# Kernel tuning notes

Hardware: AMD Instinct MI355X
Metric: run time of the kernel (lower is better)

Reference implementation:

```python
import jax, jax.numpy as jnp
import numpy as np

T = 32768   # frames
N = 1024    # notes
THRESHOLD = 0.5  # half a semitone (quarter tone) in midi norm


def setup_inputs() -> dict:
    key = jax.random.key(0)
    k1, k2 = jax.random.split(key)
    gen_f0 = jax.random.normal(k1, (T,), dtype=jnp.float32)
    t_f0 = jax.random.normal(k2, (T,), dtype=jnp.float32)
    # N non-overlapping note segments tiling the T frames: note k active on
    # [onset_k, offset_k). Equivalent to binary onset/offset event vectors of
    # length T with one onset and one offset per note.
    seg = T // N
    onset_times = jnp.arange(N, dtype=jnp.int32) * seg
    offset_times = onset_times + seg
    return {"gen_f0": gen_f0, "t_f0": t_f0,
            "onset_times": onset_times, "offset_times": offset_times}


def reference(gen_f0, t_f0, onset_times, offset_times):
    # Dense temporal mask (T, N): mask[t, k] = 1 iff onset_k <= t < offset_k.
    t = jnp.arange(gen_f0.shape[0], dtype=jnp.int32)[:, None]        # (T, 1)
    mask = ((t >= onset_times[None, :]) & (t < offset_times[None, :])
            ).astype(gen_f0.dtype)                                   # (T, N)
    # Per-note means: mean(mask*f0, 0) / mean(mask, 0) == sum(mask*f0)/sum(mask)
    msum = jnp.sum(mask, axis=0)                                      # (N,)
    mean_gen = jnp.einsum('tn,t->n', mask, gen_f0) / msum             # (N,)
    mean_ref = jnp.einsum('tn,t->n', mask, t_f0) / msum               # (N,)
    diff = jnp.abs(mean_gen - mean_ref)
    loss = jnp.mean((diff > THRESHOLD).astype(gen_f0.dtype))
    return loss
```

## Files before the change

kernel.cpp:

```cpp
#include <hip/hip_runtime.h>
#include <hip/hip_bf16.h>


#define THRESHOLD 0.5f

__global__ __launch_bounds__(1024) void pitch_loss_kernel(
    const float* __restrict__ gen,
    const float* __restrict__ tf,
    const int* __restrict__ onset,
    const int* __restrict__ offs,
    float* __restrict__ out,
    int N) {
  const int k = threadIdx.x;

  int flag = 0;
  if (k < N) {
    const int a = onset[k];
    const int b = offs[k];
    const int len = b - a;

    float sg = 0.0f, st = 0.0f;
    if (((a & 3) == 0) && ((len & 3) == 0)) {
      const float4* g4 = reinterpret_cast<const float4*>(gen + a);
      const float4* t4 = reinterpret_cast<const float4*>(tf + a);
      const int n4 = len >> 2;
      for (int i = 0; i < n4; ++i) {
        const float4 g = g4[i];
        const float4 t = t4[i];
        sg += g.x + g.y + g.z + g.w;
        st += t.x + t.y + t.z + t.w;
      }
    } else {
      for (int t = a; t < b; ++t) {
        sg += gen[t];
        st += tf[t];
      }
    }

    const float inv = 1.0f / (float)len;
    const float diff = fabsf(sg * inv - st * inv);
    flag = (diff > THRESHOLD) ? 1 : 0;
  }

  __shared__ int warp_cnt[16];
  const unsigned long long bal = __ballot(flag);
  const int wid = threadIdx.x >> 6;
  const int lane = threadIdx.x & 63;
  if (lane == 0) warp_cnt[wid] = __popcll(bal);
  __syncthreads();

  if (threadIdx.x == 0) {
    int c = 0;
    const int nw = (blockDim.x + 63) >> 6;
    for (int i = 0; i < nw; ++i) c += warp_cnt[i];
    out[0] = (float)c / (float)N;
  }
}

extern "C" void kernel_launch(void* const* d_in, const int* in_sizes, int n_in,
                              void* d_out, int out_size, void* d_ws, size_t ws_size,
                              hipStream_t stream) {
  const float* gen = (const float*)d_in[0];
  const float* tf = (const float*)d_in[1];
  const int* onset = (const int*)d_in[2];
  const int* offs = (const int*)d_in[3];
  float* out = (float*)d_out;
  const int N = in_sizes[2];

  pitch_loss_kernel<<<1, 1024, 0, stream>>>(gen, tf, onset, offs, out, N);
}
```

Measured before the change: 68.17 us.

## Spread per-note reduction across 8 lanes and many blocks with atomic finish

Instead of a single 1024-thread block where each thread serially sums a whole note segment, each note is now handled by 8 lanes with strided float4 loads and a shuffle reduction, and the grid spans many 256-thread blocks. Per-block counts are combined via atomics in a workspace buffer, with the last block writing the final loss. This removes the single-CU bottleneck and long serial loops, at the cost of a memset launch and global atomics.

```diff
diff --git a/kernel.cpp b/kernel.cpp
--- a/kernel.cpp
+++ b/kernel.cpp
@@ -4,56 +4,70 @@
 
 #define THRESHOLD 0.5f
 
-__global__ __launch_bounds__(1024) void pitch_loss_kernel(
+__global__ __launch_bounds__(256) void pitch_loss_kernel(
     const float* __restrict__ gen,
     const float* __restrict__ tf,
     const int* __restrict__ onset,
     const int* __restrict__ offs,
-    float* __restrict__ out,
-    int N) {
-  const int k = threadIdx.x;
+    int N,
+    int* __restrict__ counters,
+    float* __restrict__ out) {
+  const int tid = threadIdx.x;
+  const int g = blockIdx.x * blockDim.x + tid;
+  const int note = g >> 3;
+  const int j = g & 7;
 
   int flag = 0;
-  if (k < N) {
-    const int a = onset[k];
-    const int b = offs[k];
+  if (note < N) {
+    const int a = onset[note];
+    const int b = offs[note];
     const int len = b - a;
 
     float sg = 0.0f, st = 0.0f;
     if (((a & 3) == 0) && ((len & 3) == 0)) {
-      const float4* g4 = reinterpret_cast<const float4*>(gen + a);
-      const float4* t4 = reinterpret_cast<const float4*>(tf + a);
-      const int n4 = len >> 2;
-      for (int i = 0; i < n4; ++i) {
-        const float4 g = g4[i];
-        const float4 t = t4[i];
-        sg += g.x + g.y + g.z + g.w;
-        st += t.x + t.y + t.z + t.w;
+      for (int idx = a + (j << 2); idx + 3 < b; idx += 32) {
+        const float4 gv = *reinterpret_cast<const float4*>(gen + idx);
+        const float4 tv = *reinterpret_cast<const float4*>(tf + idx);
+        sg += gv.x + gv.y + gv.z + gv.w;
+        st += tv.x + tv.y + tv.z + tv.w;
       }
     } else {
-      for (int t = a; t < b; ++t) {
-        sg += gen[t];
-        st += tf[t];
+      for (int idx = a + j; idx < b; idx += 8) {
+        sg += gen[idx];
+        st += tf[idx];
       }
     }
 
-    const float inv = 1.0f / (float)len;
-    const float diff = fabsf(sg * inv - st * inv);
-    flag = (diff > THRESHOLD) ? 1 : 0;
+    for (int d = 1; d < 8; d <<= 1) {
+      sg += __shfl_xor(sg, d, 64);
+      st += __shfl_xor(st, d, 64);
+    }
+
+    if (j == 0) {
+      const float inv = 1.0f / (float)len;
+      const float diff = fabsf(sg * inv - st * inv);
+      flag = (diff > THRESHOLD) ? 1 : 0;
+    }
   }
 
-  __shared__ int warp_cnt[16];
+  __shared__ int warp_cnt[4];
   const unsigned long long bal = __ballot(flag);
-  const int wid = threadIdx.x >> 6;
-  const int lane = threadIdx.x & 63;
+  const int wid = tid >> 6;
+  const int lane = tid & 63;
   if (lane == 0) warp_cnt[wid] = __popcll(bal);
   __syncthreads();
 
-  if (threadIdx.x == 0) {
-    int c = 0;
+  if (tid == 0) {
+    int c = warp_cnt[0];
     const int nw = (blockDim.x + 63) >> 6;
-    for (int i = 0; i < nw; ++i) c += warp_cnt[i];
-    out[0] = (float)c / (float)N;
+    for (int i = 1; i < nw; ++i) c += warp_cnt[i];
+    atomicAdd(&counters[0], c);
+    __threadfence();
+    const int t = atomicAdd(&counters[1], 1);
+    if (t == (int)gridDim.x - 1) {
+      const int total = atomicAdd(&counters[0], 0);
+      out[0] = (float)total / (float)N;
+    }
   }
 }
 
@@ -67,5 +81,12 @@
   float* out = (float*)d_out;
   const int N = in_sizes[2];
 
-  pitch_loss_kernel<<<1, 1024, 0, stream>>>(gen, tf, onset, offs, out, N);
+  int* counters = (int*)d_ws;
+  hipMemsetAsync(counters, 0, 2 * sizeof(int), stream);
+
+  const int threads_needed = N * 8;
+  const int block = 256;
+  const int grid = (threads_needed + block - 1) / block;
+  pitch_loss_kernel<<<grid, block, 0, stream>>>(gen, tf, onset, offs, N,
+                                                counters, out);
 }
```

Result: faster. 61.72 us (-9.5%).
